# Kernel tuning notes

Hardware: AMD Instinct MI355X
Metric: run time of the kernel (lower is better)

## Reference

```python
import jax, jax.numpy as jnp
import numpy as np

N_NODES = 50000
N_FEAT = 512
N_HID = 128
N_CLASS = 8
N_EDGES = 640000


def setup_inputs() -> dict:
    key = jax.random.key(0)
    k1, k2, k3, k4, k5 = jax.random.split(key, 5)
    x = jax.random.normal(k1, (N_NODES, N_FEAT), dtype=jnp.float32)
    edge_index = jax.random.randint(k2, (2, N_EDGES), 0, N_NODES, dtype=jnp.int64)
    # GCNConv linear weight (glorot), stored as [nfeat, nhid] for x @ W
    s_conv = jnp.sqrt(6.0 / (N_FEAT + N_HID)).astype(jnp.float32)
    W_conv = jax.random.uniform(k3, (N_FEAT, N_HID), jnp.float32, -s_conv, s_conv)
    b_conv = jnp.zeros((N_HID,), jnp.float32)
    # fc head, xavier_uniform per weights_init, bias zero
    s_fc = jnp.sqrt(6.0 / (N_HID + N_CLASS)).astype(jnp.float32)
    W_fc = jax.random.uniform(k4, (N_HID, N_CLASS), jnp.float32, -s_fc, s_fc)
    b_fc = jnp.zeros((N_CLASS,), jnp.float32)
    return {"x": x, "edge_index": edge_index, "W_conv": W_conv,
            "b_conv": b_conv, "W_fc": W_fc, "b_fc": b_fc}


def reference(x, edge_index, W_conv, b_conv, W_fc, b_fc):
    N = x.shape[0]
    # GCNConv: add self-loops, symmetric normalization deg^-1/2 A deg^-1/2
    loop = jnp.arange(N, dtype=edge_index.dtype)
    src = jnp.concatenate([edge_index[0], loop])  # [E+N]
    dst = jnp.concatenate([edge_index[1], loop])
    ones = jnp.ones(src.shape[0], dtype=x.dtype)
    deg = jax.ops.segment_sum(ones, dst, num_segments=N)  # in-degree incl. self loop
    dinv = jnp.where(deg > 0, jax.lax.rsqrt(deg), 0.0)
    norm = dinv[src] * dinv[dst]  # [E+N]
    h = x @ W_conv  # [N, nhid] dense transform before propagation
    msg = h[src] * norm[:, None]  # gather + scale, [E+N, nhid]
    out = jax.ops.segment_sum(msg, dst, num_segments=N) + b_conv  # scatter-add
    # linear classification head
    return out @ W_fc + b_fc  # [N, nclass]
```

## Files before the change

kernel.cpp:

```cpp
#include <hip/hip_runtime.h>
#include <hip/hip_bf16.h>

#define NFEAT 512
#define NCLS 8
#define NHID 128
#define NPB 16
#define NBIN 3125
#define NBIN16 3136
#define WINE 1024
#define NW 625
#define BINCAP 320
#define NODECAP 64
#define NTILES 3125

typedef float4 f4;
typedef unsigned short u16;
typedef unsigned int u32;
typedef short bf16x8 __attribute__((ext_vector_type(8)));
typedef float f32x4 __attribute__((ext_vector_type(4)));

__device__ inline u16 f2bf(float f) {
    __hip_bfloat16 h = __float2bfloat16(f);
    u16 u; __builtin_memcpy(&u, &h, 2);
    return u;
}

__global__ __launch_bounds__(256) void histinit_kernel(
    const int* __restrict__ dst,
    const float* __restrict__ W1, const float* __restrict__ W2,
    const float* __restrict__ b1, const float* __restrict__ b2,
    u16* __restrict__ WbT, float* __restrict__ bias2,
    int* __restrict__ wincnt, int E)
{
    const int tid = threadIdx.x;
    const int bid = blockIdx.x;
    int t = bid * 256 + tid;
    if (t < NFEAT * NCLS) {
        int k = t >> 3, c = t & 7;
        const float* w1r = W1 + k * NHID;
        float acc = 0.f;
        #pragma unroll 8
        for (int j = 0; j < NHID; ++j) acc = fmaf(w1r[j], W2[j * NCLS + c], acc);
        WbT[c * NFEAT + k] = f2bf(acc);
        WbT[(c + 8) * NFEAT + k] = 0;
    }
    if (t < NCLS) {
        float acc = b2[t];
        for (int j = 0; j < NHID; ++j) acc = fmaf(b1[j], W2[j * NCLS + t], acc);
        bias2[t] = acc;
    }

    __shared__ int hist[NBIN16];
    for (int k = tid; k < NBIN16; k += 256) hist[k] = 0;
    __syncthreads();
    int e0 = bid * WINE;
    #pragma unroll
    for (int j = 0; j < 4; ++j) {
        int e = e0 + j * 256 + tid;
        if (e < E) atomicAdd(&hist[dst[e] >> 4], 1);
    }
    __syncthreads();
    int* row = wincnt + (size_t)bid * NBIN16;
    for (int k = tid; k < NBIN16; k += 256) row[k] = hist[k];
}

__global__ __launch_bounds__(256) void colprefix_kernel(
    int* __restrict__ wincnt, int* __restrict__ colsum)
{
    const int bg = blockIdx.x;
    const int t = threadIdx.x;
    const int bl = t & 15, chunk = t >> 4;
    const int CPW = (NW + 15) / 16;
    int vals[40];
    int s = 0;
    for (int k = 0; k < CPW; ++k) {
        int win = chunk * CPW + k;
        int v = (win < NW) ? wincnt[(size_t)win * NBIN16 + bg * 16 + bl] : 0;
        vals[k] = v; s += v;
    }
    __shared__ int part[256];
    part[bl * 16 + chunk] = s;
    __syncthreads();
    int base = 0;
    for (int c = 0; c < chunk; ++c) base += part[bl * 16 + c];
    int run = base;
    for (int k = 0; k < CPW; ++k) {
        int win = chunk * CPW + k;
        if (win < NW) {
            wincnt[(size_t)win * NBIN16 + bg * 16 + bl] = run;
            run += vals[k];
        }
    }
    if (chunk == 15) colsum[bg * 16 + bl] = run;
}

__global__ __launch_bounds__(256) void passgemm_kernel(
    const int* __restrict__ src, const int* __restrict__ dst,
    const float* __restrict__ x, const u16* __restrict__ WbT,
    const int* __restrict__ wincnt, u32* __restrict__ ebuf,
    float* __restrict__ g, int N, int E)
{
    const int tid  = threadIdx.x;
    const int bid  = blockIdx.x;
    const int lane = tid & 63;
    const int wid  = bid * 4 + (tid >> 6);
    const int r16  = lane & 15;
    const int g4   = lane >> 4;

    __shared__ int loff[NBIN16];
    __shared__ int rank[NBIN16];

    auto do_pass = [&]() {
        if (bid >= NW) return;
        const int* row = wincnt + (size_t)bid * NBIN16;
        for (int k = tid; k < NBIN16; k += 256) {
            loff[k] = row[k];
            rank[k] = 0;
        }
        __syncthreads();
        int e0 = bid * WINE;
        #pragma unroll
        for (int j = 0; j < 4; ++j) {
            int e = e0 + j * 256 + tid;
            if (e < E) {
                int d = dst[e];
                int b = d >> 4;
                int r = atomicAdd(&rank[b], 1);
                int pos = loff[b] + r;
                if (pos < BINCAP) {
                    u32 val = (u32)src[e] | ((u32)(d & 15) << 16);
                    __builtin_nontemporal_store(val, &ebuf[(size_t)b * BINCAP + pos]);
                }
            }
        }
    };

    auto do_gemm = [&]() {
        if (wid >= NTILES) return;
        const int row0 = wid * 16;
        const float* xr = x + (size_t)(row0 + r16) * NFEAT + g4 * 8;
        const u16*   wp = WbT + r16 * NFEAT + g4 * 8;
        f32x4 acc = {0.f, 0.f, 0.f, 0.f};
        #pragma unroll
        for (int ks = 0; ks < NFEAT / 32; ++ks) {
            f4 p = *(const f4*)(xr + ks * 32);
            f4 q = *(const f4*)(xr + ks * 32 + 4);
            union { bf16x8 v; u16 u[8]; } af;
            af.u[0] = f2bf(p.x); af.u[1] = f2bf(p.y);
            af.u[2] = f2bf(p.z); af.u[3] = f2bf(p.w);
            af.u[4] = f2bf(q.x); af.u[5] = f2bf(q.y);
            af.u[6] = f2bf(q.z); af.u[7] = f2bf(q.w);
            bf16x8 bv = *(const bf16x8*)(wp + ks * 32);
            acc = __builtin_amdgcn_mfma_f32_16x16x32_bf16(af.v, bv, acc, 0, 0, 0);
        }
        if (r16 < NCLS) {
            #pragma unroll
            for (int r = 0; r < 4; ++r)
                g[(size_t)(row0 + g4 * 4 + r) * 8 + r16] = acc[r];
        }
    };

    if (bid & 1) { do_pass(); do_gemm(); }
    else         { do_gemm(); do_pass(); }
}

__global__ __launch_bounds__(256) void degscale_kernel(
    const u32* __restrict__ ebuf, const int* __restrict__ colsum,
    float* __restrict__ g)
{
    const int tid = threadIdx.x;
    const int wv = tid >> 6, lane = tid & 63;
    const int bin = blockIdx.x * 4 + wv;
    if (bin >= NBIN) return;
    __shared__ int cnt_s[4][NPB];
    if (lane < NPB) cnt_s[wv][lane] = 0;
    __syncthreads();
    int cnt = min(colsum[bin], BINCAP);
    const u32* eb = ebuf + (size_t)bin * BINCAP;
    for (int k = lane; k < cnt; k += 64)
        atomicAdd(&cnt_s[wv][eb[k] >> 16], 1);
    __syncthreads();
    #pragma unroll
    for (int half = 0; half < 2; ++half) {
        int k2 = lane + half * 64;
        int node = k2 >> 3, c = k2 & 7;
        int i = bin * NPB + node;
        float di = rsqrtf((float)cnt_s[wv][node] + 1.0f);
        g[(size_t)i * 8 + c] *= di;
    }
}

__global__ __launch_bounds__(256) void gather_kernel(
    const u32* __restrict__ ebuf, const int* __restrict__ colsum,
    const float* __restrict__ g, const float* __restrict__ bias2,
    float* __restrict__ out)
{
    const int tid = threadIdx.x;
    const int wv = tid >> 6, lane = tid & 63;
    const int bin = blockIdx.x * 4 + wv;
    if (bin >= NBIN) return;
    __shared__ u16 list[4][NPB][NODECAP];
    __shared__ int cnt_s[4][NPB];
    if (lane < NPB) cnt_s[wv][lane] = 0;
    __syncthreads();
    int cnt = min(colsum[bin], BINCAP);
    const u32* eb = ebuf + (size_t)bin * BINCAP;
    for (int k = lane; k < cnt; k += 64) {
        u32 u = eb[k];
        int node = u >> 16;
        int r = atomicAdd(&cnt_s[wv][node], 1);
        if (r < NODECAP) list[wv][node][r] = (u16)(u & 0xFFFF);
    }
    __syncthreads();
    #pragma unroll
    for (int half = 0; half < 2; ++half) {
        int k2 = lane + half * 64;
        int node = k2 >> 3, c = k2 & 7;
        int i = bin * NPB + node;
        int n = min(cnt_s[wv][node], NODECAP);
        float acc = 0.f;
        for (int k = 0; k < n; ++k) {
            int s = list[wv][node][k];
            acc += g[(size_t)s * 8 + c];
        }
        float di = rsqrtf((float)cnt_s[wv][node] + 1.0f);
        out[(size_t)i * 8 + c] = fmaf(di, acc + g[(size_t)i * 8 + c], bias2[c]);
    }
}

extern "C" void kernel_launch(void* const* d_in, const int* in_sizes, int n_in,
                              void* d_out, int out_size, void* d_ws, size_t ws_size,
                              hipStream_t stream)
{
    const float* x  = (const float*)d_in[0];
    const int*   ei = (const int*)d_in[1];
    const float* W1 = (const float*)d_in[2];
    const float* b1 = (const float*)d_in[3];
    const float* W2 = (const float*)d_in[4];
    const float* b2 = (const float*)d_in[5];
    float* out = (float*)d_out;

    const int N = in_sizes[0] / NFEAT;
    const int E = in_sizes[1] / 2;
    const int* src = ei;
    const int* dst = ei + E;

    char* ws = (char*)d_ws;
    size_t off = 0;
    auto alloc = [&](size_t bytes) {
        char* p = ws + off;
        off += (bytes + 255) & ~(size_t)255;
        return p;
    };
    int*   wincnt = (int*)alloc((size_t)NW * NBIN16 * 4);
    int*   colsum = (int*)alloc((size_t)NBIN16 * 4);
    u32*   ebuf   = (u32*)alloc((size_t)NBIN * BINCAP * 4);
    float* g      = (float*)alloc((size_t)N * 8 * 4);
    u16*   WbT    = (u16*)alloc((size_t)16 * NFEAT * 2);
    float* bias2  = (float*)alloc(NCLS * 4);

    const int FB = 782;
    const int BB = (NBIN + 3) / 4;

    histinit_kernel<<<NW, 256, 0, stream>>>(dst, W1, W2, b1, b2, WbT, bias2, wincnt, E);

    colprefix_kernel<<<196, 256, 0, stream>>>(wincnt, colsum);

    passgemm_kernel<<<FB, 256, 0, stream>>>(src, dst, x, WbT, wincnt, ebuf, g, N, E);

    degscale_kernel<<<BB, 256, 0, stream>>>(ebuf, colsum, g);

    gather_kernel<<<BB, 256, 0, stream>>>(ebuf, colsum, g, bias2, out);
}
```

Measured before the change: 72.24 us.

## Split GEMM K dimension across two waves and reduce partials in degscale

The x@W projection now splits each 16-row tile's 512-wide K reduction into two halves handled by separate waves, which doubles the grid to raise memory-level parallelism for streaming x. Each half writes its partial into its own buffer, and degscale sums the two partials before applying the degree scale. The GEMM loop also prefetches the next x chunk into registers, and the launch bounds request higher occupancy. In exchange it adds two extra N×8 partial buffers and their extra reads and writes, and removes the alternating pass/gemm ordering inside blocks.

```diff
diff --git a/kernel.cpp b/kernel.cpp
--- a/kernel.cpp
+++ b/kernel.cpp
@@ -11,7 +11,7 @@
 #define NW 625
 #define BINCAP 320
 #define NODECAP 64
-#define NTILES 3125
+#define NHT 6250
 
 typedef float4 f4;
 typedef unsigned short u16;
@@ -94,24 +94,22 @@
     if (chunk == 15) colsum[bg * 16 + bl] = run;
 }
 
-__global__ __launch_bounds__(256) void passgemm_kernel(
+__global__ __launch_bounds__(256, 6) void mainfused_kernel(
     const int* __restrict__ src, const int* __restrict__ dst,
     const float* __restrict__ x, const u16* __restrict__ WbT,
     const int* __restrict__ wincnt, u32* __restrict__ ebuf,
-    float* __restrict__ g, int N, int E)
+    float* __restrict__ gp0, float* __restrict__ gp1, int N, int E)
 {
     const int tid  = threadIdx.x;
     const int bid  = blockIdx.x;
     const int lane = tid & 63;
-    const int wid  = bid * 4 + (tid >> 6);
     const int r16  = lane & 15;
     const int g4   = lane >> 4;
 
     __shared__ int loff[NBIN16];
     __shared__ int rank[NBIN16];
 
-    auto do_pass = [&]() {
-        if (bid >= NW) return;
+    if (bid < NW) {
         const int* row = wincnt + (size_t)bid * NBIN16;
         for (int k = tid; k < NBIN16; k += 256) {
             loff[k] = row[k];
@@ -133,39 +131,48 @@
                 }
             }
         }
-    };
-
-    auto do_gemm = [&]() {
-        if (wid >= NTILES) return;
-        const int row0 = wid * 16;
-        const float* xr = x + (size_t)(row0 + r16) * NFEAT + g4 * 8;
-        const u16*   wp = WbT + r16 * NFEAT + g4 * 8;
-        f32x4 acc = {0.f, 0.f, 0.f, 0.f};
+    }
+
+    const int ht = bid * 4 + (tid >> 6);
+    if (ht >= NHT) return;
+    const int tile = ht >> 1;
+    const int half = ht & 1;
+    const int row0 = tile * 16;
+    const int k0   = half * 256;
+
+    const float* xr = x + (size_t)(row0 + r16) * NFEAT + k0 + g4 * 8;
+    const u16*   wp = WbT + r16 * NFEAT + k0 + g4 * 8;
+
+    f32x4 acc = {0.f, 0.f, 0.f, 0.f};
+    f4 p = *(const f4*)(xr);
+    f4 q = *(const f4*)(xr + 4);
+    #pragma unroll
+    for (int ks = 0; ks < 8; ++ks) {
+        f4 pn, qn;
+        if (ks < 7) {
+            pn = *(const f4*)(xr + (ks + 1) * 32);
+            qn = *(const f4*)(xr + (ks + 1) * 32 + 4);
+        }
+        union { bf16x8 v; u16 u[8]; } af;
+        af.u[0] = f2bf(p.x); af.u[1] = f2bf(p.y);
+        af.u[2] = f2bf(p.z); af.u[3] = f2bf(p.w);
+        af.u[4] = f2bf(q.x); af.u[5] = f2bf(q.y);
+        af.u[6] = f2bf(q.z); af.u[7] = f2bf(q.w);
+        bf16x8 bv = *(const bf16x8*)(wp + ks * 32);
+        acc = __builtin_amdgcn_mfma_f32_16x16x32_bf16(af.v, bv, acc, 0, 0, 0);
+        if (ks < 7) { p = pn; q = qn; }
+    }
+    float* gp = half ? gp1 : gp0;
+    if (r16 < NCLS) {
         #pragma unroll
-        for (int ks = 0; ks < NFEAT / 32; ++ks) {
-            f4 p = *(const f4*)(xr + ks * 32);
-            f4 q = *(const f4*)(xr + ks * 32 + 4);
-            union { bf16x8 v; u16 u[8]; } af;
-            af.u[0] = f2bf(p.x); af.u[1] = f2bf(p.y);
-            af.u[2] = f2bf(p.z); af.u[3] = f2bf(p.w);
-            af.u[4] = f2bf(q.x); af.u[5] = f2bf(q.y);
-            af.u[6] = f2bf(q.z); af.u[7] = f2bf(q.w);
-            bf16x8 bv = *(const bf16x8*)(wp + ks * 32);
-            acc = __builtin_amdgcn_mfma_f32_16x16x32_bf16(af.v, bv, acc, 0, 0, 0);
-        }
-        if (r16 < NCLS) {
-            #pragma unroll
-            for (int r = 0; r < 4; ++r)
-                g[(size_t)(row0 + g4 * 4 + r) * 8 + r16] = acc[r];
-        }
-    };
-
-    if (bid & 1) { do_pass(); do_gemm(); }
-    else         { do_gemm(); do_pass(); }
+        for (int r = 0; r < 4; ++r)
+            gp[(size_t)(row0 + g4 * 4 + r) * 8 + r16] = acc[r];
+    }
 }
 
 __global__ __launch_bounds__(256) void degscale_kernel(
     const u32* __restrict__ ebuf, const int* __restrict__ colsum,
+    const float* __restrict__ gp0, const float* __restrict__ gp1,
     float* __restrict__ g)
 {
     const int tid = threadIdx.x;
@@ -184,9 +191,9 @@
     for (int half = 0; half < 2; ++half) {
         int k2 = lane + half * 64;
         int node = k2 >> 3, c = k2 & 7;
-        int i = bin * NPB + node;
+        size_t i = (size_t)(bin * NPB + node) * 8 + c;
         float di = rsqrtf((float)cnt_s[wv][node] + 1.0f);
-        g[(size_t)i * 8 + c] *= di;
+        g[i] = (gp0[i] + gp1[i]) * di;
     }
 }
 
@@ -255,20 +262,22 @@
     int*   wincnt = (int*)alloc((size_t)NW * NBIN16 * 4);
     int*   colsum = (int*)alloc((size_t)NBIN16 * 4);
     u32*   ebuf   = (u32*)alloc((size_t)NBIN * BINCAP * 4);
+    float* gp0    = (float*)alloc((size_t)N * 8 * 4);
+    float* gp1    = (float*)alloc((size_t)N * 8 * 4);
     float* g      = (float*)alloc((size_t)N * 8 * 4);
     u16*   WbT    = (u16*)alloc((size_t)16 * NFEAT * 2);
     float* bias2  = (float*)alloc(NCLS * 4);
 
-    const int FB = 782;
+    const int MB = (NHT + 3) / 4;
     const int BB = (NBIN + 3) / 4;
 
     histinit_kernel<<<NW, 256, 0, stream>>>(dst, W1, W2, b1, b2, WbT, bias2, wincnt, E);
 
     colprefix_kernel<<<196, 256, 0, stream>>>(wincnt, colsum);
 
-    passgemm_kernel<<<FB, 256, 0, stream>>>(src, dst, x, WbT, wincnt, ebuf, g, N, E);
-
-    degscale_kernel<<<BB, 256, 0, stream>>>(ebuf, colsum, g);
+    mainfused_kernel<<<MB, 256, 0, stream>>>(src, dst, x, WbT, wincnt, ebuf, gp0, gp1, N, E);
+
+    degscale_kernel<<<BB, 256, 0, stream>>>(ebuf, colsum, gp0, gp1, g);
 
     gather_kernel<<<BB, 256, 0, stream>>>(ebuf, colsum, g, bias2, out);
 }
```

After: 79.05 us. 1.09x slower.

## Split blocks into GEMM and pass roles with coalesced LDS-staged x tiles

Applied to the files above, without the earlier changes.

Blocks of the fused pass/GEMM kernel now each take a single role: 5 of every 9 blocks run the GEMM and 4 run the edge binning pass. Before, every block did both roles in sequence. GEMM waves now load their 16x512 x tile with fully coalesced float4 reads, convert it to bf16 into an XOR-swizzled LDS buffer, and feed MFMA from LDS instead of issuing strided per-row global reads. The change aims to improve DRAM coalescing on the dominant x read and to spread the two workloads across more blocks. In exchange it uses 64KB of shared memory per block, which limits occupancy.

```diff
diff --git a/kernel.cpp b/kernel.cpp
--- a/kernel.cpp
+++ b/kernel.cpp
@@ -94,7 +94,7 @@
     if (chunk == 15) colsum[bg * 16 + bl] = run;
 }
 
-__global__ __launch_bounds__(256) void passgemm_kernel(
+__global__ __launch_bounds__(256, 2) void megafused_kernel(
     const int* __restrict__ src, const int* __restrict__ dst,
     const float* __restrict__ x, const u16* __restrict__ WbT,
     const int* __restrict__ wincnt, u32* __restrict__ ebuf,
@@ -103,22 +103,62 @@
     const int tid  = threadIdx.x;
     const int bid  = blockIdx.x;
     const int lane = tid & 63;
-    const int wid  = bid * 4 + (tid >> 6);
+    const int wv   = tid >> 6;
     const int r16  = lane & 15;
     const int g4   = lane >> 4;
 
-    __shared__ int loff[NBIN16];
-    __shared__ int rank[NBIN16];
-
-    auto do_pass = [&]() {
-        if (bid >= NW) return;
-        const int* row = wincnt + (size_t)bid * NBIN16;
+    __shared__ u16 atile[4][8192];
+
+    const int grp = bid / 9, rem = bid % 9;
+
+    if (rem < 5) {
+        const int tile = (grp * 5 + rem) * 4 + wv;
+        if (tile >= NTILES) return;
+        u16* at = &atile[wv][0];
+
+        const f4* xt = (const f4*)(x + (size_t)tile * 16 * NFEAT);
+        #pragma unroll
+        for (int i0 = 0; i0 < 32; i0 += 8) {
+            f4 v[8];
+            #pragma unroll
+            for (int j = 0; j < 8; ++j) v[j] = xt[(i0 + j) * 64 + lane];
+            #pragma unroll
+            for (int j = 0; j < 8; ++j) {
+                int idx = (i0 + j) * 64 + lane;
+                int row = idx >> 7;
+                int byteoff = (row * 1024 + (idx & 127) * 8) ^ ((row & 7) << 4);
+                u32 lo = ((u32)f2bf(v[j].y) << 16) | f2bf(v[j].x);
+                u32 hi = ((u32)f2bf(v[j].w) << 16) | f2bf(v[j].z);
+                *(uint2*)((char*)at + byteoff) = make_uint2(lo, hi);
+            }
+        }
+
+        const u16* wpb = WbT + r16 * NFEAT + g4 * 8;
+        f32x4 acc = {0.f, 0.f, 0.f, 0.f};
+        #pragma unroll
+        for (int ks = 0; ks < 16; ++ks) {
+            int byteoff = (r16 * 1024 + ks * 64 + g4 * 16) ^ ((r16 & 7) << 4);
+            bf16x8 av = *(const bf16x8*)((const char*)at + byteoff);
+            bf16x8 bv = *(const bf16x8*)(wpb + ks * 32);
+            acc = __builtin_amdgcn_mfma_f32_16x16x32_bf16(av, bv, acc, 0, 0, 0);
+        }
+        if (r16 < NCLS) {
+            #pragma unroll
+            for (int r = 0; r < 4; ++r)
+                g[(size_t)(tile * 16 + g4 * 4 + r) * 8 + r16] = acc[r];
+        }
+    } else {
+        const int win = grp * 4 + (rem - 5);
+        if (win >= NW) return;
+        int* loff = (int*)&atile[0][0];
+        int* rank = loff + NBIN16;
+        const int* row = wincnt + (size_t)win * NBIN16;
         for (int k = tid; k < NBIN16; k += 256) {
             loff[k] = row[k];
             rank[k] = 0;
         }
         __syncthreads();
-        int e0 = bid * WINE;
+        int e0 = win * WINE;
         #pragma unroll
         for (int j = 0; j < 4; ++j) {
             int e = e0 + j * 256 + tid;
@@ -133,35 +173,7 @@
                 }
             }
         }
-    };
-
-    auto do_gemm = [&]() {
-        if (wid >= NTILES) return;
-        const int row0 = wid * 16;
-        const float* xr = x + (size_t)(row0 + r16) * NFEAT + g4 * 8;
-        const u16*   wp = WbT + r16 * NFEAT + g4 * 8;
-        f32x4 acc = {0.f, 0.f, 0.f, 0.f};
-        #pragma unroll
-        for (int ks = 0; ks < NFEAT / 32; ++ks) {
-            f4 p = *(const f4*)(xr + ks * 32);
-            f4 q = *(const f4*)(xr + ks * 32 + 4);
-            union { bf16x8 v; u16 u[8]; } af;
-            af.u[0] = f2bf(p.x); af.u[1] = f2bf(p.y);
-            af.u[2] = f2bf(p.z); af.u[3] = f2bf(p.w);
-            af.u[4] = f2bf(q.x); af.u[5] = f2bf(q.y);
-            af.u[6] = f2bf(q.z); af.u[7] = f2bf(q.w);
-            bf16x8 bv = *(const bf16x8*)(wp + ks * 32);
-            acc = __builtin_amdgcn_mfma_f32_16x16x32_bf16(af.v, bv, acc, 0, 0, 0);
-        }
-        if (r16 < NCLS) {
-            #pragma unroll
-            for (int r = 0; r < 4; ++r)
-                g[(size_t)(row0 + g4 * 4 + r) * 8 + r16] = acc[r];
-        }
-    };
-
-    if (bid & 1) { do_pass(); do_gemm(); }
-    else         { do_gemm(); do_pass(); }
+    }
 }
 
 __global__ __launch_bounds__(256) void degscale_kernel(
@@ -184,9 +196,9 @@
     for (int half = 0; half < 2; ++half) {
         int k2 = lane + half * 64;
         int node = k2 >> 3, c = k2 & 7;
-        int i = bin * NPB + node;
+        size_t i = (size_t)(bin * NPB + node) * 8 + c;
         float di = rsqrtf((float)cnt_s[wv][node] + 1.0f);
-        g[(size_t)i * 8 + c] *= di;
+        g[i] *= di;
     }
 }
 
@@ -259,14 +271,14 @@
     u16*   WbT    = (u16*)alloc((size_t)16 * NFEAT * 2);
     float* bias2  = (float*)alloc(NCLS * 4);
 
-    const int FB = 782;
+    const int MB = 157 * 9;
     const int BB = (NBIN + 3) / 4;
 
     histinit_kernel<<<NW, 256, 0, stream>>>(dst, W1, W2, b1, b2, WbT, bias2, wincnt, E);
 
     colprefix_kernel<<<196, 256, 0, stream>>>(wincnt, colsum);
 
-    passgemm_kernel<<<FB, 256, 0, stream>>>(src, dst, x, WbT, wincnt, ebuf, g, N, E);
+    megafused_kernel<<<MB, 256, 0, stream>>>(src, dst, x, WbT, wincnt, ebuf, g, N, E);
 
     degscale_kernel<<<BB, 256, 0, stream>>>(ebuf, colsum, g);
 
```

New measurement: 74.80 us. 3.5% more time.
